# Kernel optimization log

Hardware: AMD Instinct MI355X
Metric: run time of the kernel (lower is better)

## Reference

```python
import jax, jax.numpy as jnp
import numpy as np

N = 100000
E = 1600000
F_IN = 128
HID = 128
OUT = 256


def setup_inputs() -> dict:
    key = jax.random.key(0)
    ks = jax.random.split(key, 8)
    node_features = jax.random.normal(ks[0], (N, F_IN), dtype=jnp.float32)
    edge_index = jax.random.randint(ks[1], (2, E), 0, N, dtype=jnp.int64)
    s = 0.05
    W1 = jax.random.normal(ks[2], (F_IN, HID), dtype=jnp.float32) * s
    b1 = jnp.zeros((HID,), dtype=jnp.float32)
    W2 = jax.random.normal(ks[3], (HID, HID), dtype=jnp.float32) * s
    b2 = jnp.zeros((HID,), dtype=jnp.float32)
    # note: source's Linear(hidden_dim, output_dim) is inconsistent with the
    # 2*hidden concat of mean+max pool; we size fc as [2*HID, OUT] so it runs.
    fcW = jax.random.normal(ks[4], (2 * HID, OUT), dtype=jnp.float32) * s
    fcb = jnp.zeros((OUT,), dtype=jnp.float32)
    return {"node_features": node_features, "edge_index": edge_index,
            "W1": W1, "b1": b1, "W2": W2, "b2": b2, "fcW": fcW, "fcb": fcb}


def _gcn_norm(edge_index, num_nodes):
    # add self loops, compute symmetric normalization (PyG GCNConv default)
    loops = jnp.arange(num_nodes, dtype=edge_index.dtype)
    src = jnp.concatenate([edge_index[0], loops])
    dst = jnp.concatenate([edge_index[1], loops])
    ones = jnp.ones(src.shape[0], dtype=jnp.float32)
    deg = jax.ops.segment_sum(ones, dst, num_segments=num_nodes)  # [N]
    dinv = jnp.where(deg > 0, jax.lax.rsqrt(deg), 0.0)
    norm = dinv[src] * dinv[dst]  # [E+N]
    return src, dst, norm


def _gcn_conv(x, W, b, src, dst, norm, num_nodes):
    h = x @ W                                     # [N, H] dense transform
    msg = h[src] * norm[:, None]                  # gather + per-edge scale
    out = jax.ops.segment_sum(msg, dst, num_segments=num_nodes)  # scatter-add
    return out + b


def reference(node_features, edge_index, W1, b1, W2, b2, fcW, fcb):
    num_nodes = node_features.shape[0]
    src, dst, norm = _gcn_norm(edge_index, num_nodes)
    x = jax.nn.relu(_gcn_conv(node_features, W1, b1, src, dst, norm, num_nodes))
    x = jax.nn.relu(_gcn_conv(x, W2, b2, src, dst, norm, num_nodes))
    # batch vector is all zeros -> single graph: global mean + max pool
    pooled = jnp.concatenate([jnp.mean(x, axis=0, keepdims=True),
                              jnp.max(x, axis=0, keepdims=True)], axis=1)  # [1, 2H]
    # dropout is identity at inference
    return pooled @ fcW + fcb  # [1, OUT]
```

## Files before the change

kernel.cpp:

```cpp
#include <hip/hip_runtime.h>
#include <hip/hip_bf16.h>
#include <hip/hip_fp16.h>

static constexpr int FDIM = 128;
static constexpr int NBKT = 1024;

typedef _Float16 h8 __attribute__((ext_vector_type(8)));
typedef _Float16 h2 __attribute__((ext_vector_type(2)));
typedef float v4f __attribute__((ext_vector_type(4)));


__global__ __launch_bounds__(256) void k_zero_init(int* __restrict__ counts,
                                                   float* __restrict__ colsum,
                                                   float* __restrict__ colmax,
                                                   int n) {
    int i = blockIdx.x * 256 + threadIdx.x;
    if (i < n) counts[i] = 0;
    if (i < FDIM) { colsum[i] = 0.0f; colmax[i] = 0.0f; }
}

__global__ __launch_bounds__(256) void k_hist(const int* __restrict__ dst,
                                              int* __restrict__ counts, int ne) {
    int i = blockIdx.x * 256 + threadIdx.x;
    if (i < ne) atomicAdd(&counts[dst[i]], 1);
}

__global__ __launch_bounds__(256) void k_dinv(const int* __restrict__ counts,
                                              float* __restrict__ dinv, int n) {
    int i = blockIdx.x * 256 + threadIdx.x;
    if (i < n) dinv[i] = 1.0f / sqrtf(1.0f + (float)counts[i]);
}


__global__ __launch_bounds__(256) void k_scan1(const int* __restrict__ counts,
                                               int* __restrict__ work,
                                               int* __restrict__ partials, int n) {
    __shared__ int tmp[256];
    int i = blockIdx.x * 256 + threadIdx.x;
    int v = (i < n) ? counts[i] : 0;
    tmp[threadIdx.x] = v;
    __syncthreads();
    for (int off = 1; off < 256; off <<= 1) {
        int t = (threadIdx.x >= off) ? tmp[threadIdx.x - off] : 0;
        __syncthreads();
        tmp[threadIdx.x] += t;
        __syncthreads();
    }
    if (i < n) work[i] = tmp[threadIdx.x] - v;
    if (threadIdx.x == 255) partials[blockIdx.x] = tmp[255];
}

__global__ __launch_bounds__(512) void k_scan2(int* __restrict__ partials, int nb) {
    __shared__ int tmp[512];
    int v = (threadIdx.x < nb) ? partials[threadIdx.x] : 0;
    tmp[threadIdx.x] = v;
    __syncthreads();
    for (int off = 1; off < 512; off <<= 1) {
        int t = (threadIdx.x >= off) ? tmp[threadIdx.x - off] : 0;
        __syncthreads();
        tmp[threadIdx.x] += t;
        __syncthreads();
    }
    if (threadIdx.x < nb) partials[threadIdx.x] = tmp[threadIdx.x] - v;
}

__global__ __launch_bounds__(256) void k_scan3(int* __restrict__ work,
                                               const int* __restrict__ partials, int n) {
    int i = blockIdx.x * 256 + threadIdx.x;
    if (i < n) work[i] += partials[blockIdx.x];
}


__global__ __launch_bounds__(1024) void k_bcur(const int* __restrict__ work,
                                               int* __restrict__ bucketCur, int n) {
    int b = threadIdx.x;
    int node = b << 7;
    bucketCur[b] = (node < n) ? work[node] : 0;
}


__global__ __launch_bounds__(256) void k_binfill(const int* __restrict__ src,
                                                 const int* __restrict__ dst,
                                                 int* __restrict__ bucketCur,
                                                 unsigned long long* __restrict__ ebuf,
                                                 int ne) {
    __shared__ int lcnt[NBKT];
    __shared__ int lbase[NBKT];
    const int e0 = blockIdx.x * 4096;
    for (int j = threadIdx.x; j < NBKT; j += 256) lcnt[j] = 0;
    __syncthreads();

    int dcache[16];
#pragma unroll
    for (int i = 0; i < 16; i++) {
        int e = e0 + i * 256 + threadIdx.x;
        int d = (e < ne) ? dst[e] : -1;
        dcache[i] = d;
        if (d >= 0) atomicAdd(&lcnt[d >> 7], 1);
    }
    __syncthreads();

    for (int j = threadIdx.x; j < NBKT; j += 256) {
        int c = lcnt[j];
        lbase[j] = c ? atomicAdd(&bucketCur[j], c) : 0;
        lcnt[j] = 0;
    }
    __syncthreads();

#pragma unroll
    for (int i = 0; i < 16; i++) {
        int e = e0 + i * 256 + threadIdx.x;
        if (e < ne) {
            int d = dcache[i];
            int s = src[e];
            int b = d >> 7;
            int lp = atomicAdd(&lcnt[b], 1);
            ebuf[lbase[b] + lp] =
                ((unsigned long long)(unsigned)d << 32) | (unsigned)s;
        }
    }
}


__global__ __launch_bounds__(256) void k_bucketfill(const unsigned long long* __restrict__ ebuf,
                                                    const int* __restrict__ work,
                                                    int* __restrict__ csr,
                                                    int n, int ne) {
    __shared__ int cur[128];
    const int b = blockIdx.x;
    const int base = b << 7;
    const int nodes = min(128, n - base);
    if (threadIdx.x < nodes) cur[threadIdx.x] = work[base + threadIdx.x];
    __syncthreads();
    const int beg = work[base];
    const int endn = base + 128;
    const int end = (endn < n) ? work[endn] : ne;
    for (int i = beg + threadIdx.x; i < end; i += 256) {
        unsigned long long p = ebuf[i];
        int d = (int)(p >> 32);
        int s = (int)(p & 0xffffffffu);
        int pos = atomicAdd(&cur[d & 127], 1);
        csr[pos] = s;
    }
}


__global__ __launch_bounds__(256) void k_transW(const float* __restrict__ W1,
                                                const float* __restrict__ W2,
                                                _Float16* __restrict__ T1,
                                                _Float16* __restrict__ T2) {
    int b = blockIdx.x;
    const float* W = (b < 64) ? W1 : W2;
    _Float16* T = (b < 64) ? T1 : T2;
    int idx = (b & 63) * 256 + threadIdx.x;
    int k = idx >> 7, nn = idx & 127;
    T[nn * FDIM + k] = (_Float16)W[idx];
}


template <typename T>
__global__ __launch_bounds__(256) void k_gemm_f16(const T* __restrict__ X,
                                                  const _Float16* __restrict__ WT,
                                                  const float* __restrict__ dinv,
                                                  _Float16* __restrict__ H, int n) {
    __shared__ _Float16 sA[FDIM * FDIM];
    __shared__ _Float16 sB[FDIM * FDIM];
    const int t = threadIdx.x;
    const int lane = t & 63;
    const int w = t >> 6;
    const int rowhalf = w >> 1, colhalf = w & 1;

    for (int i = 0; i < 8; i++) {
        int f = i * 256 + t;
        int nn = f >> 4, g = f & 15;
        ((float4*)sB)[nn * 16 + ((g ^ nn) & 15)] = ((const float4*)WT)[f];
    }

    const int ntiles = (n + 127) >> 7;
    for (int tile = blockIdx.x; tile < ntiles; tile += gridDim.x) {
        const int R0 = tile << 7;
        __syncthreads();
        for (int i = 0; i < 8; i++) {
            int f = i * 256 + t;
            int row = f >> 4, g = f & 15;
            int gr = min(R0 + row, n - 1);
            h8 val;
            if constexpr (sizeof(T) == 4) {
                const float4* xp = (const float4*)(X + (size_t)gr * FDIM + g * 8);
                float4 u0 = xp[0], u1 = xp[1];
                val[0] = (_Float16)u0.x; val[1] = (_Float16)u0.y;
                val[2] = (_Float16)u0.z; val[3] = (_Float16)u0.w;
                val[4] = (_Float16)u1.x; val[5] = (_Float16)u1.y;
                val[6] = (_Float16)u1.z; val[7] = (_Float16)u1.w;
            } else {
                val = ((const h8*)(X + (size_t)gr * FDIM))[g];
            }
            ((h8*)sA)[row * 16 + ((g ^ row) & 15)] = val;
        }
        __syncthreads();

        v4f acc[4][4];
#pragma unroll
        for (int rt = 0; rt < 4; rt++)
#pragma unroll
            for (int ct = 0; ct < 4; ct++)
                acc[rt][ct] = (v4f){0.f, 0.f, 0.f, 0.f};

#pragma unroll
        for (int s = 0; s < 4; s++) {
            const int g0 = s * 4 + (lane >> 4);
            h8 af[4], bf[4];
#pragma unroll
            for (int rt = 0; rt < 4; rt++) {
                int row = rowhalf * 64 + rt * 16 + (lane & 15);
                af[rt] = ((const h8*)sA)[row * 16 + ((g0 ^ row) & 15)];
            }
#pragma unroll
            for (int ct = 0; ct < 4; ct++) {
                int nn = colhalf * 64 + ct * 16 + (lane & 15);
                bf[ct] = ((const h8*)sB)[nn * 16 + ((g0 ^ nn) & 15)];
            }
#pragma unroll
            for (int rt = 0; rt < 4; rt++)
#pragma unroll
                for (int ct = 0; ct < 4; ct++)
                    acc[rt][ct] = __builtin_amdgcn_mfma_f32_16x16x32_f16(
                        af[rt], bf[ct], acc[rt][ct], 0, 0, 0);
        }

        const int rb = R0 + rowhalf * 64 + (lane >> 4) * 4;
        const int cb = colhalf * 64 + (lane & 15);
#pragma unroll
        for (int rt = 0; rt < 4; rt++)
#pragma unroll
            for (int reg = 0; reg < 4; reg++) {
                int grow = rb + rt * 16 + reg;
                if (grow < n) {
                    float d = dinv[grow];
                    _Float16* hp = H + (size_t)grow * FDIM + cb;
#pragma unroll
                    for (int ct = 0; ct < 4; ct++)
                        hp[ct * 16] = (_Float16)(acc[rt][ct][reg] * d);
                }
            }
    }
}


__global__ __launch_bounds__(256) void k_aggregate(const int* __restrict__ work,
                                                   const int* __restrict__ csr,
                                                   const float* __restrict__ dinv,
                                                   const _Float16* __restrict__ hs,
                                                   const float* __restrict__ bias,
                                                   _Float16* __restrict__ out,
                                                   int n, int ne) {
    const int lane = threadIdx.x & 63;
    const int nwaves = gridDim.x * 4;
    int wid = (blockIdx.x * 256 + threadIdx.x) >> 6;
    const h2* hs2 = (const h2*)hs;
    const float2 bb = ((const float2*)bias)[lane];

    for (int node = wid; node < n; node += nwaves) {
        int beg = work[node];
        int end = (node + 1 < n) ? work[node + 1] : ne;
        float dd = dinv[node];
        h2 hv = hs2[(size_t)node * 64 + lane];
        float ax = (float)hv[0];
        float ay = (float)hv[1];
        for (int chunk = beg; chunk < end; chunk += 64) {
            int m = end - chunk; if (m > 64) m = 64;
            int myidx = (lane < m) ? csr[chunk + lane] : 0;
            int j = 0;
            for (; j + 4 <= m; j += 4) {
                int s0 = __shfl(myidx, j + 0);
                int s1 = __shfl(myidx, j + 1);
                int s2 = __shfl(myidx, j + 2);
                int s3 = __shfl(myidx, j + 3);
                h2 v0 = hs2[(size_t)s0 * 64 + lane];
                h2 v1 = hs2[(size_t)s1 * 64 + lane];
                h2 v2 = hs2[(size_t)s2 * 64 + lane];
                h2 v3 = hs2[(size_t)s3 * 64 + lane];
                ax += (float)v0[0] + (float)v1[0] + (float)v2[0] + (float)v3[0];
                ay += (float)v0[1] + (float)v1[1] + (float)v2[1] + (float)v3[1];
            }
            for (; j < m; j++) {
                int s = __shfl(myidx, j);
                h2 v = hs2[(size_t)s * 64 + lane];
                ax += (float)v[0];
                ay += (float)v[1];
            }
        }
        float ox = fmaxf(ax * dd + bb.x, 0.f);
        float oy = fmaxf(ay * dd + bb.y, 0.f);
        h2 o; o[0] = (_Float16)ox; o[1] = (_Float16)oy;
        ((h2*)out)[(size_t)node * 64 + lane] = o;
    }
}


__global__ __launch_bounds__(256) void k_pool_h(const _Float16* __restrict__ X,
                                                float* __restrict__ colsum,
                                                float* __restrict__ colmax, int n) {
    __shared__ float ls[256], lm[256];
    int c = threadIdx.x & 127;
    int grp = threadIdx.x >> 7;
    float s = 0.f, m = 0.f;
    for (int r = blockIdx.x * 2 + grp; r < n; r += gridDim.x * 2) {
        float v = (float)X[(size_t)r * FDIM + c];
        s += v;
        m = fmaxf(m, v);
    }
    ls[threadIdx.x] = s;
    lm[threadIdx.x] = m;
    __syncthreads();
    if (threadIdx.x < 128) {
        s = ls[threadIdx.x] + ls[threadIdx.x + 128];
        m = fmaxf(lm[threadIdx.x], lm[threadIdx.x + 128]);
        unsafeAtomicAdd(&colsum[c], s);
        atomicMax((int*)colmax + c, __float_as_int(m));
    }
}

__global__ __launch_bounds__(256) void k_pool_f(const float* __restrict__ X,
                                                float* __restrict__ colsum,
                                                float* __restrict__ colmax, int n) {
    __shared__ float ls[256], lm[256];
    int c = threadIdx.x & 127;
    int grp = threadIdx.x >> 7;
    float s = 0.f, m = 0.f;
    for (int r = blockIdx.x * 2 + grp; r < n; r += gridDim.x * 2) {
        float v = X[(size_t)r * FDIM + c];
        s += v;
        m = fmaxf(m, v);
    }
    ls[threadIdx.x] = s;
    lm[threadIdx.x] = m;
    __syncthreads();
    if (threadIdx.x < 128) {
        s = ls[threadIdx.x] + ls[threadIdx.x + 128];
        m = fmaxf(lm[threadIdx.x], lm[threadIdx.x + 128]);
        unsafeAtomicAdd(&colsum[c], s);
        atomicMax((int*)colmax + c, __float_as_int(m));
    }
}

__global__ __launch_bounds__(256) void k_fc(const float* __restrict__ colsum,
                                            const float* __restrict__ colmax,
                                            const float* __restrict__ fcW,
                                            const float* __restrict__ fcb,
                                            float* __restrict__ out, float invN) {
    int o = threadIdx.x;
    float acc = fcb[o];
#pragma unroll 4
    for (int k = 0; k < FDIM; k++)
        acc += colsum[k] * invN * fcW[k * 256 + o];
#pragma unroll 4
    for (int k = 0; k < FDIM; k++)
        acc += colmax[k] * fcW[(FDIM + k) * 256 + o];
    out[o] = acc;
}


__global__ __launch_bounds__(256) void k_initF(float* deg, float* cs, float* cm, int n) {
    int i = blockIdx.x * 256 + threadIdx.x;
    if (i < n) deg[i] = 1.0f;
    if (i < FDIM) { cs[i] = 0.0f; cm[i] = 0.0f; }
}
__global__ __launch_bounds__(256) void k_degreeF(const int* dst, float* deg, int ne) {
    int i = blockIdx.x * 256 + threadIdx.x;
    if (i < ne) unsafeAtomicAdd(&deg[dst[i]], 1.0f);
}
__global__ __launch_bounds__(256) void k_rsqrtF(float* deg, int n) {
    int i = blockIdx.x * 256 + threadIdx.x;
    if (i < n) deg[i] = 1.0f / sqrtf(deg[i]);
}
__global__ __launch_bounds__(256) void k_selfinitF(const float* H, const float* dinv,
                                                   float* acc, int n) {
    int i = blockIdx.x * 256 + threadIdx.x;
    if (i >= n * 32) return;
    int row = i >> 5;
    float s = dinv[row]; s *= s;
    float4 v = ((const float4*)H)[i];
    v.x *= s; v.y *= s; v.z *= s; v.w *= s;
    ((float4*)acc)[i] = v;
}
__global__ __launch_bounds__(256) void k_scatterF(const int* src, const int* dst,
                                                  const float* dinv, const float* H,
                                                  float* acc, int ne) {
    int e = (blockIdx.x * 256 + threadIdx.x) >> 6;
    if (e >= ne) return;
    int lane = threadIdx.x & 63;
    int s = src[e], d = dst[e];
    float w = dinv[s] * dinv[d];
    float2 v = ((const float2*)(H + (size_t)s * FDIM))[lane];
    float* ap = acc + (size_t)d * FDIM + lane * 2;
    unsafeAtomicAdd(ap, v.x * w);
    unsafeAtomicAdd(ap + 1, v.y * w);
}
__global__ __launch_bounds__(256) void k_bias_reluF(float* acc, const float* b, int n) {
    int i = blockIdx.x * 256 + threadIdx.x;
    if (i >= n * 32) return;
    float4 bb = ((const float4*)b)[i & 31];
    float4 v = ((float4*)acc)[i];
    v.x = fmaxf(v.x + bb.x, 0.f);
    v.y = fmaxf(v.y + bb.y, 0.f);
    v.z = fmaxf(v.z + bb.z, 0.f);
    v.w = fmaxf(v.w + bb.w, 0.f);
    ((float4*)acc)[i] = v;
}
__global__ __launch_bounds__(256) void k_gemm128F(const float* X, const float* W,
                                                   float* H, int n) {
    __shared__ float sW[FDIM * FDIM];
    for (int i = threadIdx.x; i < FDIM * FDIM / 4; i += 256)
        ((float4*)sW)[i] = ((const float4*)W)[i];
    __syncthreads();
    const int c = threadIdx.x & 127;
    const int half = threadIdx.x >> 7;
    for (int base = blockIdx.x * 8; base < n; base += gridDim.x * 8) {
        const int r0 = base + half * 4;
        const float* xp0 = X + (size_t)min(r0 + 0, n - 1) * FDIM;
        const float* xp1 = X + (size_t)min(r0 + 1, n - 1) * FDIM;
        const float* xp2 = X + (size_t)min(r0 + 2, n - 1) * FDIM;
        const float* xp3 = X + (size_t)min(r0 + 3, n - 1) * FDIM;
        float a0 = 0.f, a1 = 0.f, a2 = 0.f, a3 = 0.f;
#pragma unroll 8
        for (int k = 0; k < FDIM; k += 4) {
            float w0 = sW[(k + 0) * FDIM + c];
            float w1 = sW[(k + 1) * FDIM + c];
            float w2 = sW[(k + 2) * FDIM + c];
            float w3 = sW[(k + 3) * FDIM + c];
            float4 x0 = *(const float4*)(xp0 + k);
            float4 x1 = *(const float4*)(xp1 + k);
            float4 x2 = *(const float4*)(xp2 + k);
            float4 x3 = *(const float4*)(xp3 + k);
            a0 += x0.x * w0 + x0.y * w1 + x0.z * w2 + x0.w * w3;
            a1 += x1.x * w0 + x1.y * w1 + x1.z * w2 + x1.w * w3;
            a2 += x2.x * w0 + x2.y * w1 + x2.z * w2 + x2.w * w3;
            a3 += x3.x * w0 + x3.y * w1 + x3.z * w2 + x3.w * w3;
        }
        if (r0 + 0 < n) H[(size_t)(r0 + 0) * FDIM + c] = a0;
        if (r0 + 1 < n) H[(size_t)(r0 + 1) * FDIM + c] = a1;
        if (r0 + 2 < n) H[(size_t)(r0 + 2) * FDIM + c] = a2;
        if (r0 + 3 < n) H[(size_t)(r0 + 3) * FDIM + c] = a3;
    }
}


extern "C" void kernel_launch(void* const* d_in, const int* in_sizes, int n_in,
                              void* d_out, int out_size, void* d_ws, size_t ws_size,
                              hipStream_t stream) {
    const float* X   = (const float*)d_in[0];
    const int*   ei  = (const int*)d_in[1];
    const float* W1  = (const float*)d_in[2];
    const float* b1  = (const float*)d_in[3];
    const float* W2  = (const float*)d_in[4];
    const float* b2  = (const float*)d_in[5];
    const float* fcW = (const float*)d_in[6];
    const float* fcb = (const float*)d_in[7];
    float* out = (float*)d_out;

    const int n  = in_sizes[0] / FDIM;
    const int ne = in_sizes[1] / 2;
    const int* src = ei;
    const int* dst = ei + ne;

    const int gN = (n + 255) / 256;
    const int gE = (ne + 255) / 256;
    const int nbkt = (n + 127) >> 7;
    const int gB = (ne + 4095) / 4096;

    size_t need = (size_t)ne * 8 + (size_t)n * FDIM * 2 * 2 + 2 * FDIM * FDIM * 2 +
                  ((size_t)n + 2 * FDIM) * 4 +
                  ((size_t)n * 2 + 512 + NBKT + ne) * 4;

    if (ws_size >= need && gN <= 512 && nbkt <= NBKT) {
        unsigned long long* ebuf = (unsigned long long*)d_ws;
        _Float16* h    = (_Float16*)(ebuf + ne);
        _Float16* xbuf = h + (size_t)n * FDIM;
        _Float16* w1t  = xbuf + (size_t)n * FDIM;
        _Float16* w2t  = w1t + FDIM * FDIM;
        float* dinv    = (float*)(w2t + FDIM * FDIM);
        float* colsum  = dinv + n;
        float* colmax  = colsum + FDIM;
        int* counts    = (int*)(colmax + FDIM);
        int* work      = counts + n;
        int* partials  = work + n;
        int* bucketCur = partials + 512;
        int* csr       = bucketCur + NBKT;

        k_zero_init<<<gN, 256, 0, stream>>>(counts, colsum, colmax, n);
        k_hist<<<gE, 256, 0, stream>>>(dst, counts, ne);
        k_dinv<<<gN, 256, 0, stream>>>(counts, dinv, n);
        k_scan1<<<gN, 256, 0, stream>>>(counts, work, partials, n);
        k_scan2<<<1, 512, 0, stream>>>(partials, gN);
        k_scan3<<<gN, 256, 0, stream>>>(work, partials, n);
        k_bcur<<<1, NBKT, 0, stream>>>(work, bucketCur, n);
        k_binfill<<<gB, 256, 0, stream>>>(src, dst, bucketCur, ebuf, ne);
        k_bucketfill<<<nbkt, 256, 0, stream>>>(ebuf, work, csr, n, ne);
        k_transW<<<128, 256, 0, stream>>>(W1, W2, w1t, w2t);

        k_gemm_f16<float><<<512, 256, 0, stream>>>(X, w1t, dinv, h, n);
        k_aggregate<<<2048, 256, 0, stream>>>(work, csr, dinv, h, b1, xbuf, n, ne);
        k_gemm_f16<_Float16><<<512, 256, 0, stream>>>(xbuf, w2t, dinv, h, n);
        k_aggregate<<<2048, 256, 0, stream>>>(work, csr, dinv, h, b2, xbuf, n, ne);

        k_pool_h<<<1024, 256, 0, stream>>>(xbuf, colsum, colmax, n);
        k_fc<<<1, 256, 0, stream>>>(colsum, colmax, fcW, fcb, out, 1.0f / (float)n);
    } else {
        float* h      = (float*)d_ws;
        float* acc    = h + (size_t)n * FDIM;
        float* dinv   = acc + (size_t)n * FDIM;
        float* colsum = dinv + n;
        float* colmax = colsum + FDIM;
        const int gV = (n * 32 + 255) / 256;
        const int gS = (int)(((long long)ne * 64 + 255) / 256);

        k_initF<<<gN, 256, 0, stream>>>(dinv, colsum, colmax, n);
        k_degreeF<<<gE, 256, 0, stream>>>(dst, dinv, ne);
        k_rsqrtF<<<gN, 256, 0, stream>>>(dinv, n);

        k_gemm128F<<<1024, 256, 0, stream>>>(X, W1, h, n);
        k_selfinitF<<<gV, 256, 0, stream>>>(h, dinv, acc, n);
        k_scatterF<<<gS, 256, 0, stream>>>(src, dst, dinv, h, acc, ne);
        k_bias_reluF<<<gV, 256, 0, stream>>>(acc, b1, n);

        k_gemm128F<<<1024, 256, 0, stream>>>(acc, W2, h, n);
        k_selfinitF<<<gV, 256, 0, stream>>>(h, dinv, acc, n);
        k_scatterF<<<gS, 256, 0, stream>>>(src, dst, dinv, h, acc, ne);
        k_bias_reluF<<<gV, 256, 0, stream>>>(acc, b2, n);

        k_pool_f<<<1024, 256, 0, stream>>>(acc, colsum, colmax, n);
        k_fc<<<1, 256, 0, stream>>>(colsum, colmax, fcW, fcb, out, 1.0f / (float)n);
    }
}
```

Before: 437.5 us.

## Replace per-node global histogram and scan with bucket-level histogram and in-bucket counting

Removes the per-node global atomic histogram, the three-pass node scan, and the bucket-cursor kernel. Edges are now counted per coarse bucket of 128 nodes with shared-memory histograms over 128 blocks, followed by a single-block scan over the buckets. The bucket processing kernel now builds the per-node counts, offsets and dinv in shared memory before scattering into the CSR array. This cuts the kernel count and the contended global atomics, but each bucket's edges are read twice and the bin-fill blocks now handle twice as many edges each.

```diff
diff --git a/kernel.cpp b/kernel.cpp
--- a/kernel.cpp
+++ b/kernel.cpp
@@ -4,80 +4,51 @@
 
 static constexpr int FDIM = 128;
 static constexpr int NBKT = 1024;
+static constexpr int BHB = 128;
 
 typedef _Float16 h8 __attribute__((ext_vector_type(8)));
 typedef _Float16 h2 __attribute__((ext_vector_type(2)));
 typedef float v4f __attribute__((ext_vector_type(4)));
 
 
-__global__ __launch_bounds__(256) void k_zero_init(int* __restrict__ counts,
-                                                   float* __restrict__ colsum,
-                                                   float* __restrict__ colmax,
-                                                   int n) {
-    int i = blockIdx.x * 256 + threadIdx.x;
-    if (i < n) counts[i] = 0;
+__global__ __launch_bounds__(256) void k_zero128(float* __restrict__ colsum,
+                                                 float* __restrict__ colmax) {
+    int i = threadIdx.x;
     if (i < FDIM) { colsum[i] = 0.0f; colmax[i] = 0.0f; }
 }
 
-__global__ __launch_bounds__(256) void k_hist(const int* __restrict__ dst,
-                                              int* __restrict__ counts, int ne) {
-    int i = blockIdx.x * 256 + threadIdx.x;
-    if (i < ne) atomicAdd(&counts[dst[i]], 1);
-}
-
-__global__ __launch_bounds__(256) void k_dinv(const int* __restrict__ counts,
-                                              float* __restrict__ dinv, int n) {
-    int i = blockIdx.x * 256 + threadIdx.x;
-    if (i < n) dinv[i] = 1.0f / sqrtf(1.0f + (float)counts[i]);
-}
-
-
-__global__ __launch_bounds__(256) void k_scan1(const int* __restrict__ counts,
-                                               int* __restrict__ work,
-                                               int* __restrict__ partials, int n) {
-    __shared__ int tmp[256];
-    int i = blockIdx.x * 256 + threadIdx.x;
-    int v = (i < n) ? counts[i] : 0;
-    tmp[threadIdx.x] = v;
-    __syncthreads();
-    for (int off = 1; off < 256; off <<= 1) {
-        int t = (threadIdx.x >= off) ? tmp[threadIdx.x - off] : 0;
+__global__ __launch_bounds__(256) void k_bhist(const int* __restrict__ dst,
+                                               int* __restrict__ bucketPart, int ne) {
+    __shared__ int lb[NBKT];
+    for (int j = threadIdx.x; j < NBKT; j += 256) lb[j] = 0;
+    __syncthreads();
+    int stride = gridDim.x * 256;
+    for (int e = blockIdx.x * 256 + threadIdx.x; e < ne; e += stride)
+        atomicAdd(&lb[dst[e] >> 7], 1);
+    __syncthreads();
+    int* mine = bucketPart + blockIdx.x * NBKT;
+    for (int j = threadIdx.x; j < NBKT; j += 256) mine[j] = lb[j];
+}
+
+__global__ __launch_bounds__(1024) void k_scanB(const int* __restrict__ bucketPart,
+                                                int* __restrict__ bucketBase,
+                                                int* __restrict__ bucketCur) {
+    __shared__ int tmp[NBKT];
+    int t = threadIdx.x;
+    int v = 0;
+    for (int k = 0; k < BHB; k++) v += bucketPart[k * NBKT + t];
+    tmp[t] = v;
+    __syncthreads();
+    for (int off = 1; off < NBKT; off <<= 1) {
+        int u = (t >= off) ? tmp[t - off] : 0;
         __syncthreads();
-        tmp[threadIdx.x] += t;
+        tmp[t] += u;
         __syncthreads();
     }
-    if (i < n) work[i] = tmp[threadIdx.x] - v;
-    if (threadIdx.x == 255) partials[blockIdx.x] = tmp[255];
-}
-
-__global__ __launch_bounds__(512) void k_scan2(int* __restrict__ partials, int nb) {
-    __shared__ int tmp[512];
-    int v = (threadIdx.x < nb) ? partials[threadIdx.x] : 0;
-    tmp[threadIdx.x] = v;
-    __syncthreads();
-    for (int off = 1; off < 512; off <<= 1) {
-        int t = (threadIdx.x >= off) ? tmp[threadIdx.x - off] : 0;
-        __syncthreads();
-        tmp[threadIdx.x] += t;
-        __syncthreads();
-    }
-    if (threadIdx.x < nb) partials[threadIdx.x] = tmp[threadIdx.x] - v;
-}
-
-__global__ __launch_bounds__(256) void k_scan3(int* __restrict__ work,
-                                               const int* __restrict__ partials, int n) {
-    int i = blockIdx.x * 256 + threadIdx.x;
-    if (i < n) work[i] += partials[blockIdx.x];
-}
-
-
-__global__ __launch_bounds__(1024) void k_bcur(const int* __restrict__ work,
-                                               int* __restrict__ bucketCur, int n) {
-    int b = threadIdx.x;
-    int node = b << 7;
-    bucketCur[b] = (node < n) ? work[node] : 0;
-}
-
+    int excl = tmp[t] - v;
+    bucketBase[t] = excl;
+    bucketCur[t] = excl;
+}
 
 __global__ __launch_bounds__(256) void k_binfill(const int* __restrict__ src,
                                                  const int* __restrict__ dst,
@@ -86,13 +57,13 @@
                                                  int ne) {
     __shared__ int lcnt[NBKT];
     __shared__ int lbase[NBKT];
-    const int e0 = blockIdx.x * 4096;
+    const int e0 = blockIdx.x * 8192;
     for (int j = threadIdx.x; j < NBKT; j += 256) lcnt[j] = 0;
     __syncthreads();
 
-    int dcache[16];
-#pragma unroll
-    for (int i = 0; i < 16; i++) {
+    int dcache[32];
+#pragma unroll
+    for (int i = 0; i < 32; i++) {
         int e = e0 + i * 256 + threadIdx.x;
         int d = (e < ne) ? dst[e] : -1;
         dcache[i] = d;
@@ -108,7 +79,7 @@
     __syncthreads();
 
 #pragma unroll
-    for (int i = 0; i < 16; i++) {
+    for (int i = 0; i < 32; i++) {
         int e = e0 + i * 256 + threadIdx.x;
         if (e < ne) {
             int d = dcache[i];
@@ -121,25 +92,52 @@
     }
 }
 
-
-__global__ __launch_bounds__(256) void k_bucketfill(const unsigned long long* __restrict__ ebuf,
-                                                    const int* __restrict__ work,
-                                                    int* __restrict__ csr,
-                                                    int n, int ne) {
-    __shared__ int cur[128];
+__global__ __launch_bounds__(256) void k_bucketproc(const unsigned long long* __restrict__ ebuf,
+                                                    const int* __restrict__ bucketBase,
+                                                    const int* __restrict__ bucketEnd,
+                                                    int* __restrict__ work,
+                                                    float* __restrict__ dinv,
+                                                    int* __restrict__ csr, int n) {
+    __shared__ int cnt[128];
+    __shared__ int scn[128];
     const int b = blockIdx.x;
     const int base = b << 7;
-    const int nodes = min(128, n - base);
-    if (threadIdx.x < nodes) cur[threadIdx.x] = work[base + threadIdx.x];
-    __syncthreads();
-    const int beg = work[base];
-    const int endn = base + 128;
-    const int end = (endn < n) ? work[endn] : ne;
+    const int beg = bucketBase[b], end = bucketEnd[b];
+
+    if (threadIdx.x < 128) cnt[threadIdx.x] = 0;
+    __syncthreads();
+    for (int i = beg + threadIdx.x; i < end; i += 256) {
+        int d = (int)(ebuf[i] >> 32);
+        atomicAdd(&cnt[d & 127], 1);
+    }
+    __syncthreads();
+
+    int v = 0;
+    if (threadIdx.x < 128) { v = cnt[threadIdx.x]; scn[threadIdx.x] = v; }
+    __syncthreads();
+    for (int off = 1; off < 128; off <<= 1) {
+        int t = 0;
+        if (threadIdx.x < 128 && threadIdx.x >= off) t = scn[threadIdx.x - off];
+        __syncthreads();
+        if (threadIdx.x < 128) scn[threadIdx.x] += t;
+        __syncthreads();
+    }
+    if (threadIdx.x < 128) {
+        int node = base + threadIdx.x;
+        if (node < n) {
+            int w = beg + scn[threadIdx.x] - v;
+            work[node] = w;
+            dinv[node] = 1.0f / sqrtf(1.0f + (float)v);
+            cnt[threadIdx.x] = w;
+        }
+    }
+    __syncthreads();
+
     for (int i = beg + threadIdx.x; i < end; i += 256) {
         unsigned long long p = ebuf[i];
         int d = (int)(p >> 32);
         int s = (int)(p & 0xffffffffu);
-        int pos = atomicAdd(&cur[d & 127], 1);
+        int pos = atomicAdd(&cnt[d & 127], 1);
         csr[pos] = s;
     }
 }
@@ -467,13 +465,13 @@
     const int gN = (n + 255) / 256;
     const int gE = (ne + 255) / 256;
     const int nbkt = (n + 127) >> 7;
-    const int gB = (ne + 4095) / 4096;
+    const int gB = (ne + 8191) / 8192;
 
     size_t need = (size_t)ne * 8 + (size_t)n * FDIM * 2 * 2 + 2 * FDIM * FDIM * 2 +
                   ((size_t)n + 2 * FDIM) * 4 +
-                  ((size_t)n * 2 + 512 + NBKT + ne) * 4;
-
-    if (ws_size >= need && gN <= 512 && nbkt <= NBKT) {
+                  ((size_t)n + (size_t)(BHB + 2) * NBKT + ne) * 4;
+
+    if (ws_size >= need && nbkt <= NBKT) {
         unsigned long long* ebuf = (unsigned long long*)d_ws;
         _Float16* h    = (_Float16*)(ebuf + ne);
         _Float16* xbuf = h + (size_t)n * FDIM;
@@ -482,21 +480,18 @@
         float* dinv    = (float*)(w2t + FDIM * FDIM);
         float* colsum  = dinv + n;
         float* colmax  = colsum + FDIM;
-        int* counts    = (int*)(colmax + FDIM);
-        int* work      = counts + n;
-        int* partials  = work + n;
-        int* bucketCur = partials + 512;
+        int* work      = (int*)(colmax + FDIM);
+        int* bucketPart= work + n;
+        int* bucketBase= bucketPart + BHB * NBKT;
+        int* bucketCur = bucketBase + NBKT;
         int* csr       = bucketCur + NBKT;
 
-        k_zero_init<<<gN, 256, 0, stream>>>(counts, colsum, colmax, n);
-        k_hist<<<gE, 256, 0, stream>>>(dst, counts, ne);
-        k_dinv<<<gN, 256, 0, stream>>>(counts, dinv, n);
-        k_scan1<<<gN, 256, 0, stream>>>(counts, work, partials, n);
-        k_scan2<<<1, 512, 0, stream>>>(partials, gN);
-        k_scan3<<<gN, 256, 0, stream>>>(work, partials, n);
-        k_bcur<<<1, NBKT, 0, stream>>>(work, bucketCur, n);
+        k_zero128<<<1, 256, 0, stream>>>(colsum, colmax);
+        k_bhist<<<BHB, 256, 0, stream>>>(dst, bucketPart, ne);
+        k_scanB<<<1, NBKT, 0, stream>>>(bucketPart, bucketBase, bucketCur);
         k_binfill<<<gB, 256, 0, stream>>>(src, dst, bucketCur, ebuf, ne);
-        k_bucketfill<<<nbkt, 256, 0, stream>>>(ebuf, work, csr, n, ne);
+        k_bucketproc<<<nbkt, 256, 0, stream>>>(ebuf, bucketBase, bucketCur,
+                                               work, dinv, csr, n);
         k_transW<<<128, 256, 0, stream>>>(W1, W2, w1t, w2t);
 
         k_gemm_f16<float><<<512, 256, 0, stream>>>(X, w1t, dinv, h, n);
```

Result: faster. 387.8 us (-11.4%).
